# Performance work log

Measured on AMD Instinct MI355X. Metric: run time of the kernel, lower is better.

The kernel has to match this reference:

```python
import jax, jax.numpy as jnp
import numpy as np

B, N, S, C, H = 16, 64, 4096, 768, 8
HD = C // H
SCALE = HD ** -0.5
ASSIGN_EPS = 1.0


def hard_softmax(logits, axis):
    # softmax over `axis`, then straight-through one-hot argmax along `axis`
    y_soft = jax.nn.softmax(logits, axis=axis)
    idx = jnp.argmax(y_soft, axis=axis, keepdims=True)
    n = logits.shape[axis]
    shape = [1] * logits.ndim
    shape[axis] = n
    iota = jnp.arange(n).reshape(shape)
    y_hard = (iota == idx).astype(logits.dtype)
    return y_hard - jax.lax.stop_gradient(y_soft) + y_soft


def setup_inputs() -> dict:
    key = jax.random.key(0)
    ks = jax.random.split(key, 7)
    w = lambda k, shp: (jax.random.normal(k, shp, dtype=jnp.float32) * 0.02)
    return {
        'query': jax.random.normal(ks[0], (B, N, C), dtype=jnp.float32),
        'key_in': jax.random.normal(ks[1], (B, S, C), dtype=jnp.float32),
        'Wq': w(ks[2], (C, C)),
        'Wk': w(ks[3], (C, C)),
        'Wv': w(ks[4], (C, C)),
        'Wo': w(ks[5], (C, C)),
        'bo': jnp.zeros((C,), dtype=jnp.float32),
    }


def reference(query, key_in, Wq, Wk, Wv, Wo, bo):
    # linear projections (torch Linear: x @ W.T), split heads -> b h n d
    q = jnp.einsum('bnc,dc->bnd', query, Wq).reshape(B, N, H, HD).transpose(0, 2, 1, 3)
    k = jnp.einsum('bsc,dc->bsd', key_in, Wk).reshape(B, S, H, HD).transpose(0, 2, 1, 3)
    v = jnp.einsum('bsc,dc->bsd', key_in, Wv).reshape(B, S, H, HD).transpose(0, 2, 1, 3)
    raw_attn = jnp.einsum('bhnd,bhsd->bhns', q, k) * SCALE      # [B,H,N,S]
    attn = hard_softmax(raw_attn, axis=-2)                       # hard assign over groups N
    attn = attn / (attn.sum(axis=-1, keepdims=True) + ASSIGN_EPS)  # renorm over tokens S
    out = jnp.einsum('bhns,bhsd->bhnd', attn, v)                 # [B,H,N,HD]
    out = out.transpose(0, 2, 1, 3).reshape(B, N, C)
    out = jnp.einsum('bnc,dc->bnd', out, Wo) + bo
    return out
```

## Files before the change

### kernel.cpp

```cpp
#include <hip/hip_runtime.h>

#define BB 16
#define NN 64
#define SS 4096
#define CC 768
#define HH 8
#define HD 96

typedef __attribute__((ext_vector_type(8))) short bf16x8;
typedef __attribute__((ext_vector_type(4))) float f32x4;

static __device__ __forceinline__ unsigned short f2bf(float x) {
  unsigned u = __float_as_uint(x);
  unsigned r = (u + 0x7fffu + ((u >> 16) & 1u)) >> 16;
  return (unsigned short)r;
}
static __device__ __forceinline__ float bf2f(unsigned short h) {
  return __uint_as_float(((unsigned)h) << 16);
}
static __device__ __forceinline__ void split2t(float f0, float f1,
                                               unsigned* hw, unsigned* lw) {
  unsigned u0 = __float_as_uint(f0), u1 = __float_as_uint(f1);
  *hw = (u0 >> 16) | (u1 & 0xffff0000u);
  float l0 = f0 - __uint_as_float(u0 & 0xffff0000u);
  float l1 = f1 - __uint_as_float(u1 & 0xffff0000u);
  unsigned v0 = __float_as_uint(l0), v1 = __float_as_uint(l1);
  *lw = (v0 >> 16) | (v1 & 0xffff0000u);
}

__global__ __launch_bounds__(256) void k_transpose(
    const float* __restrict__ src, float* __restrict__ dst) {
  __shared__ float tile[32][33];
  const int bx = blockIdx.x % 24, by = blockIdx.x / 24;
  const int tx = threadIdx.x & 31, ty = threadIdx.x >> 5;
#pragma unroll
  for (int k = 0; k < 4; ++k)
    tile[ty + k * 8][tx] = src[(size_t)(by * 32 + ty + k * 8) * CC + bx * 32 + tx];
  __syncthreads();
#pragma unroll
  for (int k = 0; k < 4; ++k)
    dst[(size_t)(bx * 32 + ty + k * 8) * CC + by * 32 + tx] = tile[tx][ty + k * 8];
}

__global__ __launch_bounds__(256) void k_qkfold(
    const float* __restrict__ query, const float* __restrict__ WqT,
    const float* __restrict__ Wk, double* __restrict__ qk64,
    unsigned short* __restrict__ qhp, unsigned short* __restrict__ qlp) {
  __shared__ double qin[2][CC];
  __shared__ double q64[2][CC];
  const int tid = threadIdx.x;
  const int r0 = blockIdx.x * 2;

#pragma unroll
  for (int u = 0; u < 6; ++u) {
    int idx = tid + u * 256;
    int r = idx / CC, c = idx - r * CC;
    qin[r][c] = (double)query[(size_t)(r0 + r) * CC + c];
  }
  __syncthreads();

  {
    double a00 = 0.0, a01 = 0.0, a02 = 0.0;
    double a10 = 0.0, a11 = 0.0, a12 = 0.0;
    const float* wt = WqT + tid;
    for (int e = 0; e < CC; ++e) {
      const double q0 = qin[0][e], q1 = qin[1][e];
      const float* w = wt + (size_t)e * CC;
      const double w0 = (double)w[0], w1 = (double)w[256], w2 = (double)w[512];
      a00 += q0 * w0; a01 += q0 * w1; a02 += q0 * w2;
      a10 += q1 * w0; a11 += q1 * w1; a12 += q1 * w2;
    }
    q64[0][tid] = a00; q64[0][tid + 256] = a01; q64[0][tid + 512] = a02;
    q64[1][tid] = a10; q64[1][tid + 256] = a11; q64[1][tid + 512] = a12;
  }
  __syncthreads();

  const double SC = 0.10206207261596575;
  for (int h = 0; h < HH; ++h) {
    double b00 = 0.0, b01 = 0.0, b02 = 0.0;
    double b10 = 0.0, b11 = 0.0, b12 = 0.0;
    const float* wk = Wk + (size_t)(h * HD) * CC + tid;
    const double* qh0 = &q64[0][h * HD];
    const double* qh1 = &q64[1][h * HD];
#pragma unroll 4
    for (int dd = 0; dd < HD; ++dd) {
      const float* w = wk + (size_t)dd * CC;
      const double w0 = (double)w[0], w1 = (double)w[256], w2 = (double)w[512];
      const double q0 = qh0[dd], q1 = qh1[dd];
      b00 += q0 * w0; b01 += q0 * w1; b02 += q0 * w2;
      b10 += q1 * w0; b11 += q1 * w1; b12 += q1 * w2;
    }
    double av[2][3] = {{b00 * SC, b01 * SC, b02 * SC},
                       {b10 * SC, b11 * SC, b12 * SC}};
#pragma unroll
    for (int r = 0; r < 2; ++r) {
      const int row = r0 + r, b_ = row >> 6, n = row & 63;
      const int col512 = h * 64 + n;
#pragma unroll
      for (int m = 0; m < 3; ++m) {
        const int c = tid + m * 256;
        size_t o = ((size_t)(b_ * HH + h) * NN + n) * CC + c;
        qk64[o] = av[r][m];
        float f = (float)av[r][m];
        unsigned short hh16 = f2bf(f);
        const int cs = c >> 5, lkc = (c >> 3) & 3, j = c & 7;
        size_t po = (((size_t)(b_ * 24 + cs) * 32 + (col512 >> 4)) * 64 +
                     (lkc * 16 + (col512 & 15))) * 8 + j;
        qhp[po] = hh16;
        qlp[po] = f2bf(f - bf2f(hh16));
      }
    }
  }
}

#define DELTA 1e-3f

__global__ __launch_bounds__(512) void k_filter_mfma(
    const float* __restrict__ key,
    const unsigned short* __restrict__ qhp, const unsigned short* __restrict__ qlp,
    unsigned char* __restrict__ assign_t, int* __restrict__ susp,
    int* __restrict__ scnt) {
  __shared__ float alds[2][64][68];
  const int tid = threadIdx.x;
  const int lane = tid & 63;
  const int wn = tid >> 6;
  const int bid0 = blockIdx.x;
  const int swz = (bid0 & 7) * 128 + (bid0 >> 3);
  const int b = swz >> 6;
  const int s0 = (swz & 63) * 64;
  const int l16 = lane & 15;
  const int lk = lane >> 4;

  f32x4 acc[4][4];
#pragma unroll
  for (int m = 0; m < 4; ++m)
#pragma unroll
    for (int n = 0; n < 4; ++n) acc[m][n] = (f32x4){0.f, 0.f, 0.f, 0.f};

  const float* kbase = key + ((size_t)b * SS + s0) * CC;
  const int srow = tid >> 3, sc8 = tid & 7;

  const size_t bstep = (size_t)24 * 32 * 64 * 8;
  (void)bstep;
#define BBASE(cs) ((((size_t)(b * 24 + (cs)) * 32 + wn * 4) * 64 + lane) * 8)

  bf16x8 bhA[4], blA[4], bhB[4], blB[4];
  {
    float4 st0 = *(const float4*)(kbase + (size_t)srow * CC + sc8 * 8);
    float4 st1 = *(const float4*)(kbase + (size_t)srow * CC + sc8 * 8 + 4);
    *(float4*)&alds[0][srow][sc8 * 8] = st0;
    *(float4*)&alds[0][srow][sc8 * 8 + 4] = st1;
    const size_t bb = BBASE(0);
#pragma unroll
    for (int n = 0; n < 4; ++n) {
      bhA[n] = *(const bf16x8*)(qhp + bb + (size_t)n * 512);
      blA[n] = *(const bf16x8*)(qlp + bb + (size_t)n * 512);
    }
  }
  __syncthreads();

  for (int t = 0; t < 12; ++t) {
    const int cur = t & 1;
    float4 st0, st1;
    if (t < 11) {
      const int cb = (t + 1) * 64;
      st0 = *(const float4*)(kbase + (size_t)srow * CC + cb + sc8 * 8);
      st1 = *(const float4*)(kbase + (size_t)srow * CC + cb + sc8 * 8 + 4);
    }

    {
      const int cs = t * 2;
      const size_t bbn = BBASE(cs + 1);
#pragma unroll
      for (int n = 0; n < 4; ++n) {
        bhB[n] = *(const bf16x8*)(qhp + bbn + (size_t)n * 512);
        blB[n] = *(const bf16x8*)(qlp + bbn + (size_t)n * 512);
      }
      union { bf16x8 v; unsigned w[4]; } ah[4], al[4];
#pragma unroll
      for (int m = 0; m < 4; ++m) {
        const float* ap = &alds[cur][m * 16 + l16][lk * 8];
        float4 x0 = *(const float4*)ap;
        float4 x1 = *(const float4*)(ap + 4);
        split2t(x0.x, x0.y, &ah[m].w[0], &al[m].w[0]);
        split2t(x0.z, x0.w, &ah[m].w[1], &al[m].w[1]);
        split2t(x1.x, x1.y, &ah[m].w[2], &al[m].w[2]);
        split2t(x1.z, x1.w, &ah[m].w[3], &al[m].w[3]);
      }
#pragma unroll
      for (int m = 0; m < 4; ++m)
#pragma unroll
        for (int n = 0; n < 4; ++n)
          acc[m][n] = __builtin_amdgcn_mfma_f32_16x16x32_bf16(ah[m].v, bhA[n], acc[m][n], 0, 0, 0);
#pragma unroll
      for (int m = 0; m < 4; ++m)
#pragma unroll
        for (int n = 0; n < 4; ++n)
          acc[m][n] = __builtin_amdgcn_mfma_f32_16x16x32_bf16(ah[m].v, blA[n], acc[m][n], 0, 0, 0);
#pragma unroll
      for (int m = 0; m < 4; ++m)
#pragma unroll
        for (int n = 0; n < 4; ++n)
          acc[m][n] = __builtin_amdgcn_mfma_f32_16x16x32_bf16(al[m].v, bhA[n], acc[m][n], 0, 0, 0);
    }

    {
      const int cs = t * 2 + 1;
      if (t < 11) {
        const size_t bbn = BBASE(cs + 1);
#pragma unroll
        for (int n = 0; n < 4; ++n) {
          bhA[n] = *(const bf16x8*)(qhp + bbn + (size_t)n * 512);
          blA[n] = *(const bf16x8*)(qlp + bbn + (size_t)n * 512);
        }
      }
      union { bf16x8 v; unsigned w[4]; } ah[4], al[4];
#pragma unroll
      for (int m = 0; m < 4; ++m) {
        const float* ap = &alds[cur][m * 16 + l16][32 + lk * 8];
        float4 x0 = *(const float4*)ap;
        float4 x1 = *(const float4*)(ap + 4);
        split2t(x0.x, x0.y, &ah[m].w[0], &al[m].w[0]);
        split2t(x0.z, x0.w, &ah[m].w[1], &al[m].w[1]);
        split2t(x1.x, x1.y, &ah[m].w[2], &al[m].w[2]);
        split2t(x1.z, x1.w, &ah[m].w[3], &al[m].w[3]);
      }
#pragma unroll
      for (int m = 0; m < 4; ++m)
#pragma unroll
        for (int n = 0; n < 4; ++n)
          acc[m][n] = __builtin_amdgcn_mfma_f32_16x16x32_bf16(ah[m].v, bhB[n], acc[m][n], 0, 0, 0);
#pragma unroll
      for (int m = 0; m < 4; ++m)
#pragma unroll
        for (int n = 0; n < 4; ++n)
          acc[m][n] = __builtin_amdgcn_mfma_f32_16x16x32_bf16(ah[m].v, blB[n], acc[m][n], 0, 0, 0);
#pragma unroll
      for (int m = 0; m < 4; ++m)
#pragma unroll
        for (int n = 0; n < 4; ++n)
          acc[m][n] = __builtin_amdgcn_mfma_f32_16x16x32_bf16(al[m].v, bhB[n], acc[m][n], 0, 0, 0);
    }

    if (t < 11) {
      *(float4*)&alds[cur ^ 1][srow][sc8 * 8] = st0;
      *(float4*)&alds[cur ^ 1][srow][sc8 * 8 + 4] = st1;
    }
    __syncthreads();
  }
#undef BBASE

#pragma unroll
  for (int m = 0; m < 4; ++m) {
    const int tokbase = s0 + m * 16 + lk * 4;
#pragma unroll
    for (int r = 0; r < 4; ++r) {
      const int tok = tokbase + r;
      float m1 = -3.402823466e38f, m2 = -3.402823466e38f;
      int i1 = 0;
#pragma unroll
      for (int n = 0; n < 4; ++n) {
        float v = acc[m][n][r];
        int g = n * 16 + l16;
        if (v > m1) { m2 = m1; m1 = v; i1 = g; }
        else if (v > m2) m2 = v;
      }
#pragma unroll
      for (int off = 1; off <= 8; off <<= 1) {
        float om1 = __shfl_xor(m1, off);
        float om2 = __shfl_xor(m2, off);
        int oi1 = __shfl_xor(i1, off);
        if (om1 > m1 || (om1 == m1 && oi1 < i1)) {
          m2 = fmaxf(m1, fmaxf(m2, om2));
          m1 = om1; i1 = oi1;
        } else {
          m2 = fmaxf(om1, fmaxf(m2, om2));
        }
      }
      if (l16 == 0) {
        const int bh2 = b * 8 + wn;
        assign_t[((size_t)b * SS + tok) * 8 + wn] = (unsigned char)i1;
        if (m1 - m2 < DELTA) {
          int w = atomicAdd(&scnt[bh2], 1);
          susp[(size_t)bh2 * SS + w] = tok;
        }
      }
    }
  }
}

__global__ __launch_bounds__(256) void k_rescore(
    const float* __restrict__ key, const double* __restrict__ qk64,
    const int* __restrict__ susp, const int* __restrict__ scnt,
    unsigned char* __restrict__ assign_t) {
  __shared__ float krow[4][CC];
  __shared__ double l64[4][64];
  const int bh = blockIdx.x;
  const int cnt = scnt[bh];
  if (cnt == 0) return;
  const int b = bh >> 3, h = bh & 7;
  const int tid = threadIdx.x;
  const int n = tid >> 2, q = tid & 3;
  const double* qrow = qk64 + ((size_t)bh * NN + n) * CC + q * 192;

  for (int i0 = 0; i0 < cnt; i0 += 4) {
    const int nb = (cnt - i0 < 4) ? (cnt - i0) : 4;
    for (int r = 0; r < nb; ++r) {
      const int s = susp[(size_t)bh * SS + i0 + r];
      for (int u = tid; u < CC; u += 256)
        krow[r][u] = key[((size_t)b * SS + s) * CC + u];
    }
    __syncthreads();
    double a0 = 0.0, a1 = 0.0, a2 = 0.0, a3 = 0.0;
    const float* k0 = &krow[0][q * 192];
    const float* k1 = &krow[1][q * 192];
    const float* k2 = &krow[2][q * 192];
    const float* k3 = &krow[3][q * 192];
#pragma unroll 4
    for (int c = 0; c < 192; ++c) {
      const double w = qrow[c];
      a0 += w * (double)k0[c];
      a1 += w * (double)k1[c];
      a2 += w * (double)k2[c];
      a3 += w * (double)k3[c];
    }
    a0 += __shfl_xor(a0, 1); a0 += __shfl_xor(a0, 2);
    a1 += __shfl_xor(a1, 1); a1 += __shfl_xor(a1, 2);
    a2 += __shfl_xor(a2, 1); a2 += __shfl_xor(a2, 2);
    a3 += __shfl_xor(a3, 1); a3 += __shfl_xor(a3, 2);
    if (q == 0) {
      l64[0][n] = a0; l64[1][n] = a1; l64[2][n] = a2; l64[3][n] = a3;
    }
    __syncthreads();
    if (tid < nb) {
      double best = l64[tid][0];
      int bi = 0;
      for (int n2 = 1; n2 < 64; ++n2)
        if (l64[tid][n2] > best) { best = l64[tid][n2]; bi = n2; }
      const int s = susp[(size_t)bh * SS + i0 + tid];
      assign_t[((size_t)b * SS + s) * 8 + h] = (unsigned char)bi;
    }
    __syncthreads();
  }
}

__global__ __launch_bounds__(256) void k_counts(
    const unsigned char* __restrict__ assign_t, int* __restrict__ counts) {
  __shared__ int hist[64];
  const int bh = blockIdx.x;
  const int b = bh >> 3, h = bh & 7;
  const int tid = threadIdx.x;
  if (tid < 64) hist[tid] = 0;
  __syncthreads();
  for (int s = tid; s < SS; s += 256)
    atomicAdd(&hist[assign_t[((size_t)b * SS + s) * 8 + h]], 1);
  __syncthreads();
  if (tid < 64) counts[bh * 64 + tid] = hist[tid];
}

__global__ __launch_bounds__(64) void k_rank(
    const unsigned char* __restrict__ assign_t, const int* __restrict__ counts,
    int* __restrict__ offsets, int* __restrict__ perm) {
  __shared__ int base[64];
  const int bh = blockIdx.x;
  const int b = bh >> 3, h = bh & 7;
  const int lane = threadIdx.x;

  int cn = counts[bh * 64 + lane];
  int off = cn;
#pragma unroll
  for (int d = 1; d < 64; d <<= 1) {
    int t = __shfl_up(off, d);
    if (lane >= d) off += t;
  }
  off -= cn;
  offsets[bh * 64 + lane] = off;
  base[lane] = off;

  for (int c = 0; c < SS / 64; ++c) {
    const int s = c * 64 + lane;
    const int g = (int)assign_t[((size_t)b * SS + s) * 8 + h];
    unsigned long long m = ~0ull;
#pragma unroll
    for (int k = 0; k < 6; ++k) {
      unsigned long long bk = __ballot((g >> k) & 1);
      m &= ((g >> k) & 1) ? bk : ~bk;
    }
    const int leader = __ffsll((unsigned long long)m) - 1;
    const int rankin = __popcll(m & ((1ull << lane) - 1ull));
    int baseo = 0;
    if (lane == leader) {
      baseo = base[g];
      base[g] = baseo + __popcll(m);
    }
    baseo = __shfl(baseo, leader);
    perm[(size_t)bh * SS + baseo + rankin] = s;
  }
}

__global__ __launch_bounds__(64) void k_gatherp(
    const float* __restrict__ key, const int* __restrict__ perm,
    const int* __restrict__ offsets, const int* __restrict__ counts,
    float* __restrict__ gsum) {
  const int bid = blockIdx.x;
  const int bh = bid >> 6;
  const int b = bh >> 3;
  const int lane = threadIdx.x;

  const int off = offsets[bid];
  const int cnt = counts[bid];
  const int* pl = perm + (size_t)bh * SS + off;
  const float* kb = key + (size_t)b * SS * CC;

  float4 a0 = {0.f, 0.f, 0.f, 0.f}, b0 = a0, c0 = a0;
  int j = 0;
  for (; j + 1 < cnt; j += 2) {
    const int s0 = pl[j], s1 = pl[j + 1];
    const float4* k0 = (const float4*)(kb + (size_t)s0 * CC);
    const float4* k1 = (const float4*)(kb + (size_t)s1 * CC);
    float4 x0 = k0[lane], x1 = k0[lane + 64], x2 = k0[lane + 128];
    float4 y0 = k1[lane], y1 = k1[lane + 64], y2 = k1[lane + 128];
    a0.x += x0.x; a0.y += x0.y; a0.z += x0.z; a0.w += x0.w;
    b0.x += x1.x; b0.y += x1.y; b0.z += x1.z; b0.w += x1.w;
    c0.x += x2.x; c0.y += x2.y; c0.z += x2.z; c0.w += x2.w;
    a0.x += y0.x; a0.y += y0.y; a0.z += y0.z; a0.w += y0.w;
    b0.x += y1.x; b0.y += y1.y; b0.z += y1.z; b0.w += y1.w;
    c0.x += y2.x; c0.y += y2.y; c0.z += y2.z; c0.w += y2.w;
  }
  if (j < cnt) {
    const int s0 = pl[j];
    const float4* k0 = (const float4*)(kb + (size_t)s0 * CC);
    float4 x0 = k0[lane], x1 = k0[lane + 64], x2 = k0[lane + 128];
    a0.x += x0.x; a0.y += x0.y; a0.z += x0.z; a0.w += x0.w;
    b0.x += x1.x; b0.y += x1.y; b0.z += x1.z; b0.w += x1.w;
    c0.x += x2.x; c0.y += x2.y; c0.z += x2.z; c0.w += x2.w;
  }
  float4* go = (float4*)(gsum + (size_t)bid * CC);
  go[lane] = a0; go[lane + 64] = b0; go[lane + 128] = c0;
}

__global__ __launch_bounds__(256) void k_out(
    const float* __restrict__ gsum, const int* __restrict__ counts,
    const float* __restrict__ WvT, const float* __restrict__ WoT,
    const float* __restrict__ bo, float* __restrict__ out) {
  __shared__ float gs[2][HH][CC];
  __shared__ float vr[2][CC];
  const int tid = threadIdx.x;
  const int r0 = blockIdx.x * 2;

  for (int r = 0; r < 2; ++r) {
    int row = r0 + r, b = row >> 6, n = row & 63;
    for (int h = 0; h < HH; ++h) {
      const float sc = 1.f / (float)(counts[(b * HH + h) * NN + n] + 1);
      const float* src = gsum + ((size_t)(b * HH + h) * NN + n) * CC;
      for (int m = 0; m < 3; ++m)
        gs[r][h][tid + m * 256] = src[tid + m * 256] * sc;
    }
  }
  __syncthreads();

  const int h0 = tid / HD, h1 = (tid + 256) / HD, h2 = (tid + 512) / HD;
  {
    float a00 = 0.f, a01 = 0.f, a02 = 0.f;
    float a10 = 0.f, a11 = 0.f, a12 = 0.f;
    const float* wt = WvT + tid;
    for (int e4 = 0; e4 < CC / 4; ++e4) {
      const int e = e4 * 4;
      float4 g00 = *(const float4*)&gs[0][h0][e];
      float4 g01 = *(const float4*)&gs[0][h1][e];
      float4 g02 = *(const float4*)&gs[0][h2][e];
      float4 g10 = *(const float4*)&gs[1][h0][e];
      float4 g11 = *(const float4*)&gs[1][h1][e];
      float4 g12 = *(const float4*)&gs[1][h2][e];
      const float* w0p = wt + (size_t)e * CC;
      const float* w1p = wt + (size_t)(e + 1) * CC;
      const float* w2p = wt + (size_t)(e + 2) * CC;
      const float* w3p = wt + (size_t)(e + 3) * CC;
      float wa = w0p[0], wb = w0p[256], wc = w0p[512];
      a00 = fmaf(g00.x, wa, a00); a01 = fmaf(g01.x, wb, a01); a02 = fmaf(g02.x, wc, a02);
      a10 = fmaf(g10.x, wa, a10); a11 = fmaf(g11.x, wb, a11); a12 = fmaf(g12.x, wc, a12);
      wa = w1p[0]; wb = w1p[256]; wc = w1p[512];
      a00 = fmaf(g00.y, wa, a00); a01 = fmaf(g01.y, wb, a01); a02 = fmaf(g02.y, wc, a02);
      a10 = fmaf(g10.y, wa, a10); a11 = fmaf(g11.y, wb, a11); a12 = fmaf(g12.y, wc, a12);
      wa = w2p[0]; wb = w2p[256]; wc = w2p[512];
      a00 = fmaf(g00.z, wa, a00); a01 = fmaf(g01.z, wb, a01); a02 = fmaf(g02.z, wc, a02);
      a10 = fmaf(g10.z, wa, a10); a11 = fmaf(g11.z, wb, a11); a12 = fmaf(g12.z, wc, a12);
      wa = w3p[0]; wb = w3p[256]; wc = w3p[512];
      a00 = fmaf(g00.w, wa, a00); a01 = fmaf(g01.w, wb, a01); a02 = fmaf(g02.w, wc, a02);
      a10 = fmaf(g10.w, wa, a10); a11 = fmaf(g11.w, wb, a11); a12 = fmaf(g12.w, wc, a12);
    }
    vr[0][tid] = a00; vr[0][tid + 256] = a01; vr[0][tid + 512] = a02;
    vr[1][tid] = a10; vr[1][tid + 256] = a11; vr[1][tid + 512] = a12;
  }
  __syncthreads();

  {
    float a00 = bo[tid], a01 = bo[tid + 256], a02 = bo[tid + 512];
    float a10 = a00, a11 = a01, a12 = a02;
    const float* wt = WoT + tid;
    for (int e4 = 0; e4 < CC / 4; ++e4) {
      const int e = e4 * 4;
      float4 v0 = *(const float4*)&vr[0][e];
      float4 v1 = *(const float4*)&vr[1][e];
      const float* w0p = wt + (size_t)e * CC;
      const float* w1p = wt + (size_t)(e + 1) * CC;
      const float* w2p = wt + (size_t)(e + 2) * CC;
      const float* w3p = wt + (size_t)(e + 3) * CC;
      float wa = w0p[0], wb = w0p[256], wc = w0p[512];
      a00 = fmaf(v0.x, wa, a00); a01 = fmaf(v0.x, wb, a01); a02 = fmaf(v0.x, wc, a02);
      a10 = fmaf(v1.x, wa, a10); a11 = fmaf(v1.x, wb, a11); a12 = fmaf(v1.x, wc, a12);
      wa = w1p[0]; wb = w1p[256]; wc = w1p[512];
      a00 = fmaf(v0.y, wa, a00); a01 = fmaf(v0.y, wb, a01); a02 = fmaf(v0.y, wc, a02);
      a10 = fmaf(v1.y, wa, a10); a11 = fmaf(v1.y, wb, a11); a12 = fmaf(v1.y, wc, a12);
      wa = w2p[0]; wb = w2p[256]; wc = w2p[512];
      a00 = fmaf(v0.z, wa, a00); a01 = fmaf(v0.z, wb, a01); a02 = fmaf(v0.z, wc, a02);
      a10 = fmaf(v1.z, wa, a10); a11 = fmaf(v1.z, wb, a11); a12 = fmaf(v1.z, wc, a12);
      wa = w3p[0]; wb = w3p[256]; wc = w3p[512];
      a00 = fmaf(v0.w, wa, a00); a01 = fmaf(v0.w, wb, a01); a02 = fmaf(v0.w, wc, a02);
      a10 = fmaf(v1.w, wa, a10); a11 = fmaf(v1.w, wb, a11); a12 = fmaf(v1.w, wc, a12);
    }
    out[(size_t)(r0 + 0) * CC + tid] = a00;
    out[(size_t)(r0 + 0) * CC + tid + 256] = a01;
    out[(size_t)(r0 + 0) * CC + tid + 512] = a02;
    out[(size_t)(r0 + 1) * CC + tid] = a10;
    out[(size_t)(r0 + 1) * CC + tid + 256] = a11;
    out[(size_t)(r0 + 1) * CC + tid + 512] = a12;
  }
}

extern "C" void kernel_launch(void* const* d_in, const int* in_sizes, int n_in,
                              void* d_out, int out_size, void* d_ws, size_t ws_size,
                              hipStream_t stream) {
  const float* query = (const float*)d_in[0];
  const float* key   = (const float*)d_in[1];
  const float* Wq    = (const float*)d_in[2];
  const float* Wk    = (const float*)d_in[3];
  const float* Wv    = (const float*)d_in[4];
  const float* Wo    = (const float*)d_in[5];
  const float* bo    = (const float*)d_in[6];
  float* out = (float*)d_out;

  char* ws = (char*)d_ws;
  double* qk64           = (double*)(ws);
  float* gsum            = (float*)(ws);
  unsigned short* qhp    = (unsigned short*)(ws + 50331648);
  unsigned short* qlp    = (unsigned short*)(ws + 62914560);
  unsigned char* assign_t= (unsigned char*)(ws + 75497472);
  int* susp              = (int*)(ws + 76021760);
  int* scnt              = (int*)(ws + 78118912);
  int* counts            = (int*)(ws + 78119424);
  int* offsets           = (int*)(ws + 78152192);
  int* perm              = (int*)(ws + 78184960);
  float* WqT             = (float*)(ws + 80282112);
  float* WvT             = (float*)(ws + 82641408);
  float* WoT             = (float*)(ws + 85000704);

  hipMemsetAsync(scnt, 0, 512, stream);
  k_transpose<<<576, 256, 0, stream>>>(Wq, WqT);
  k_transpose<<<576, 256, 0, stream>>>(Wv, WvT);
  k_transpose<<<576, 256, 0, stream>>>(Wo, WoT);
  k_qkfold<<<512, 256, 0, stream>>>(query, WqT, Wk, qk64, qhp, qlp);
  k_filter_mfma<<<1024, 512, 0, stream>>>(key, qhp, qlp, assign_t, susp, scnt);
  k_rescore<<<128, 256, 0, stream>>>(key, qk64, susp, scnt, assign_t);
  k_counts<<<128, 256, 0, stream>>>(assign_t, counts);
  k_rank<<<128, 64, 0, stream>>>(assign_t, counts, offsets, perm);
  k_gatherp<<<8192, 64, 0, stream>>>(key, perm, offsets, counts, gsum);
  k_out<<<512, 256, 0, stream>>>(gsum, counts, WvT, WoT, bo, out);
}
```

Baseline: 968.5 us.

## Replace rank+permuted gather with LDS-atomic scatter, batch rescore 16 rows

```diff
diff --git a/kernel.cpp b/kernel.cpp
--- a/kernel.cpp
+++ b/kernel.cpp
@@ -140,8 +140,6 @@
   const float* kbase = key + ((size_t)b * SS + s0) * CC;
   const int srow = tid >> 3, sc8 = tid & 7;
 
-  const size_t bstep = (size_t)24 * 32 * 64 * 8;
-  (void)bstep;
 #define BBASE(cs) ((((size_t)(b * 24 + (cs)) * 32 + wn * 4) * 64 + lane) * 8)
 
   bf16x8 bhA[4], blA[4], bhB[4], blB[4];
@@ -167,7 +165,6 @@
       st0 = *(const float4*)(kbase + (size_t)srow * CC + cb + sc8 * 8);
       st1 = *(const float4*)(kbase + (size_t)srow * CC + cb + sc8 * 8 + 4);
     }
-
     {
       const int cs = t * 2;
       const size_t bbn = BBASE(cs + 1);
@@ -203,11 +200,9 @@
         for (int n = 0; n < 4; ++n)
           acc[m][n] = __builtin_amdgcn_mfma_f32_16x16x32_bf16(al[m].v, bhA[n], acc[m][n], 0, 0, 0);
     }
-
     {
-      const int cs = t * 2 + 1;
       if (t < 11) {
-        const size_t bbn = BBASE(cs + 1);
+        const size_t bbn = BBASE(t * 2 + 2);
 #pragma unroll
         for (int n = 0; n < 4; ++n) {
           bhA[n] = *(const bf16x8*)(qhp + bbn + (size_t)n * 512);
@@ -293,8 +288,8 @@
     const float* __restrict__ key, const double* __restrict__ qk64,
     const int* __restrict__ susp, const int* __restrict__ scnt,
     unsigned char* __restrict__ assign_t) {
-  __shared__ float krow[4][CC];
-  __shared__ double l64[4][64];
+  __shared__ float krow[16][CC];
+  __shared__ double l64[16][64];
   const int bh = blockIdx.x;
   const int cnt = scnt[bh];
   if (cnt == 0) return;
@@ -303,33 +298,40 @@
   const int n = tid >> 2, q = tid & 3;
   const double* qrow = qk64 + ((size_t)bh * NN + n) * CC + q * 192;
 
-  for (int i0 = 0; i0 < cnt; i0 += 4) {
-    const int nb = (cnt - i0 < 4) ? (cnt - i0) : 4;
+  for (int i0 = 0; i0 < cnt; i0 += 16) {
+    const int nb = (cnt - i0 < 16) ? (cnt - i0) : 16;
     for (int r = 0; r < nb; ++r) {
       const int s = susp[(size_t)bh * SS + i0 + r];
       for (int u = tid; u < CC; u += 256)
         krow[r][u] = key[((size_t)b * SS + s) * CC + u];
     }
     __syncthreads();
-    double a0 = 0.0, a1 = 0.0, a2 = 0.0, a3 = 0.0;
-    const float* k0 = &krow[0][q * 192];
-    const float* k1 = &krow[1][q * 192];
-    const float* k2 = &krow[2][q * 192];
-    const float* k3 = &krow[3][q * 192];
-#pragma unroll 4
-    for (int c = 0; c < 192; ++c) {
-      const double w = qrow[c];
-      a0 += w * (double)k0[c];
-      a1 += w * (double)k1[c];
-      a2 += w * (double)k2[c];
-      a3 += w * (double)k3[c];
-    }
-    a0 += __shfl_xor(a0, 1); a0 += __shfl_xor(a0, 2);
-    a1 += __shfl_xor(a1, 1); a1 += __shfl_xor(a1, 2);
-    a2 += __shfl_xor(a2, 1); a2 += __shfl_xor(a2, 2);
-    a3 += __shfl_xor(a3, 1); a3 += __shfl_xor(a3, 2);
+
+    double acc[16];
+#pragma unroll
+    for (int r = 0; r < 16; ++r) acc[r] = 0.0;
+    for (int c4 = 0; c4 < 48; ++c4) {
+      const double w0 = qrow[c4 * 4 + 0];
+      const double w1 = qrow[c4 * 4 + 1];
+      const double w2 = qrow[c4 * 4 + 2];
+      const double w3 = qrow[c4 * 4 + 3];
+#pragma unroll
+      for (int r = 0; r < 16; ++r) {
+        float4 k4 = *(const float4*)&krow[r][q * 192 + c4 * 4];
+        acc[r] += w0 * (double)k4.x;
+        acc[r] += w1 * (double)k4.y;
+        acc[r] += w2 * (double)k4.z;
+        acc[r] += w3 * (double)k4.w;
+      }
+    }
+#pragma unroll
+    for (int r = 0; r < 16; ++r) {
+      acc[r] += __shfl_xor(acc[r], 1);
+      acc[r] += __shfl_xor(acc[r], 2);
+    }
     if (q == 0) {
-      l64[0][n] = a0; l64[1][n] = a1; l64[2][n] = a2; l64[3][n] = a3;
+#pragma unroll
+      for (int r = 0; r < 16; ++r) l64[r][n] = acc[r];
     }
     __syncthreads();
     if (tid < nb) {
@@ -358,85 +360,44 @@
   if (tid < 64) counts[bh * 64 + tid] = hist[tid];
 }
 
-__global__ __launch_bounds__(64) void k_rank(
-    const unsigned char* __restrict__ assign_t, const int* __restrict__ counts,
-    int* __restrict__ offsets, int* __restrict__ perm) {
-  __shared__ int base[64];
-  const int bh = blockIdx.x;
-  const int b = bh >> 3, h = bh & 7;
-  const int lane = threadIdx.x;
-
-  int cn = counts[bh * 64 + lane];
-  int off = cn;
-#pragma unroll
-  for (int d = 1; d < 64; d <<= 1) {
-    int t = __shfl_up(off, d);
-    if (lane >= d) off += t;
-  }
-  off -= cn;
-  offsets[bh * 64 + lane] = off;
-  base[lane] = off;
-
-  for (int c = 0; c < SS / 64; ++c) {
-    const int s = c * 64 + lane;
-    const int g = (int)assign_t[((size_t)b * SS + s) * 8 + h];
-    unsigned long long m = ~0ull;
-#pragma unroll
-    for (int k = 0; k < 6; ++k) {
-      unsigned long long bk = __ballot((g >> k) & 1);
-      m &= ((g >> k) & 1) ? bk : ~bk;
-    }
-    const int leader = __ffsll((unsigned long long)m) - 1;
-    const int rankin = __popcll(m & ((1ull << lane) - 1ull));
-    int baseo = 0;
-    if (lane == leader) {
-      baseo = base[g];
-      base[g] = baseo + __popcll(m);
-    }
-    baseo = __shfl(baseo, leader);
-    perm[(size_t)bh * SS + baseo + rankin] = s;
-  }
-}
-
-__global__ __launch_bounds__(64) void k_gatherp(
-    const float* __restrict__ key, const int* __restrict__ perm,
-    const int* __restrict__ offsets, const int* __restrict__ counts,
+__global__ __launch_bounds__(256) void k_gather3(
+    const float* __restrict__ key, const unsigned char* __restrict__ assign_t,
     float* __restrict__ gsum) {
+  __shared__ float sums[512 * 33];
+  const int tid = threadIdx.x;
   const int bid = blockIdx.x;
-  const int bh = bid >> 6;
-  const int b = bh >> 3;
-  const int lane = threadIdx.x;
-
-  const int off = offsets[bid];
-  const int cnt = counts[bid];
-  const int* pl = perm + (size_t)bh * SS + off;
-  const float* kb = key + (size_t)b * SS * CC;
-
-  float4 a0 = {0.f, 0.f, 0.f, 0.f}, b0 = a0, c0 = a0;
-  int j = 0;
-  for (; j + 1 < cnt; j += 2) {
-    const int s0 = pl[j], s1 = pl[j + 1];
-    const float4* k0 = (const float4*)(kb + (size_t)s0 * CC);
-    const float4* k1 = (const float4*)(kb + (size_t)s1 * CC);
-    float4 x0 = k0[lane], x1 = k0[lane + 64], x2 = k0[lane + 128];
-    float4 y0 = k1[lane], y1 = k1[lane + 64], y2 = k1[lane + 128];
-    a0.x += x0.x; a0.y += x0.y; a0.z += x0.z; a0.w += x0.w;
-    b0.x += x1.x; b0.y += x1.y; b0.z += x1.z; b0.w += x1.w;
-    c0.x += x2.x; c0.y += x2.y; c0.z += x2.z; c0.w += x2.w;
-    a0.x += y0.x; a0.y += y0.y; a0.z += y0.z; a0.w += y0.w;
-    b0.x += y1.x; b0.y += y1.y; b0.z += y1.z; b0.w += y1.w;
-    c0.x += y2.x; c0.y += y2.y; c0.z += y2.z; c0.w += y2.w;
-  }
-  if (j < cnt) {
-    const int s0 = pl[j];
-    const float4* k0 = (const float4*)(kb + (size_t)s0 * CC);
-    float4 x0 = k0[lane], x1 = k0[lane + 64], x2 = k0[lane + 128];
-    a0.x += x0.x; a0.y += x0.y; a0.z += x0.z; a0.w += x0.w;
-    b0.x += x1.x; b0.y += x1.y; b0.z += x1.z; b0.w += x1.w;
-    c0.x += x2.x; c0.y += x2.y; c0.z += x2.z; c0.w += x2.w;
-  }
-  float4* go = (float4*)(gsum + (size_t)bid * CC);
-  go[lane] = a0; go[lane + 64] = b0; go[lane + 128] = c0;
+  const int b = bid / 24;
+  const int c0 = (bid - b * 24) * 32;
+
+  for (int u = tid; u < 512 * 33; u += 256) sums[u] = 0.f;
+  __syncthreads();
+
+  const int w = tid >> 6, lane = tid & 63;
+  const int t8 = lane >> 3, cq = lane & 7;
+  const float* kb = key + (size_t)b * SS * CC + c0 + cq * 4;
+  const unsigned long long* ab =
+      (const unsigned long long*)(assign_t + (size_t)b * SS * 8);
+
+  for (int i = 0; i < 128; ++i) {
+    const int s = w * 1024 + i * 8 + t8;
+    const float4 kv = *(const float4*)(kb + (size_t)s * CC);
+    const unsigned long long a8 = ab[s];
+#pragma unroll
+    for (int h = 0; h < 8; ++h) {
+      const int n = (int)((a8 >> (h * 8)) & 63);
+      float* dst = &sums[(h * 64 + n) * 33 + cq * 4];
+      atomicAdd(dst + 0, kv.x);
+      atomicAdd(dst + 1, kv.y);
+      atomicAdd(dst + 2, kv.z);
+      atomicAdd(dst + 3, kv.w);
+    }
+  }
+  __syncthreads();
+
+  for (int u = tid; u < 512 * 32; u += 256) {
+    const int hn = u >> 5, c = u & 31;
+    gsum[((size_t)b * 512 + hn) * CC + c0 + c] = sums[hn * 33 + c];
+  }
 }
 
 __global__ __launch_bounds__(256) void k_out(
@@ -549,8 +510,6 @@
   int* susp              = (int*)(ws + 76021760);
   int* scnt              = (int*)(ws + 78118912);
   int* counts            = (int*)(ws + 78119424);
-  int* offsets           = (int*)(ws + 78152192);
-  int* perm              = (int*)(ws + 78184960);
   float* WqT             = (float*)(ws + 80282112);
   float* WvT             = (float*)(ws + 82641408);
   float* WoT             = (float*)(ws + 85000704);
@@ -563,7 +522,6 @@
   k_filter_mfma<<<1024, 512, 0, stream>>>(key, qhp, qlp, assign_t, susp, scnt);
   k_rescore<<<128, 256, 0, stream>>>(key, qk64, susp, scnt, assign_t);
   k_counts<<<128, 256, 0, stream>>>(assign_t, counts);
-  k_rank<<<128, 64, 0, stream>>>(assign_t, counts, offsets, perm);
-  k_gatherp<<<8192, 64, 0, stream>>>(key, perm, offsets, counts, gsum);
+  k_gather3<<<384, 256, 0, stream>>>(key, assign_t, gsum);
   k_out<<<512, 256, 0, stream>>>(gsum, counts, WvT, WoT, bo, out);
 }
```

New measurement: 3.315 ms. 242% more time.
